# Performance work log

Measured on AMD Instinct MI355X. Metric: run time of the kernel, lower is better.

The kernel has to match this reference:

```python
import jax, jax.numpy as jnp
import numpy as np

N_NODES = 10000
N_EDGES = 320000
S_IN, V_IN = 128, 64          # node irreps 128x0e + 64x1e
ATTR, NB = 64, 32             # node-attr scalars, radial basis size
HEADS, SH, VH = 4, 32, 16     # heads, scalars/head, l=1 vectors/head
FC = 64
S_TP, V_TP = S_IN + V_IN, S_IN + 2 * V_IN   # dtp out: 192x0e + 256x1e
NW = 2 * S_IN + 3 * V_IN                    # 448 TP path weights


def _smooth_leaky(x, alpha=0.2):
    return 0.5 * (1 + alpha) * x + 0.5 * (1 - alpha) * x * (2 * jax.nn.sigmoid(x) - 1)


def _dtp(s, v, y0, y1, w):
    """Depthwise CG tensor product of (s:0e, v:1e) with sh (y0:0e, y1:1e).
    w: [E, 448] per-edge weights or [448] internal weights."""
    w_ss = w[..., :S_IN]
    w_sv = w[..., S_IN:2 * S_IN]
    w_vs = w[..., 2 * S_IN:2 * S_IN + V_IN]
    w_dt = w[..., 2 * S_IN + V_IN:2 * S_IN + 2 * V_IN]
    w_cr = w[..., 2 * S_IN + 2 * V_IN:]
    o0a = w_ss * s * y0                                   # 0e x 0e -> 0e
    o0b = w_dt * jnp.einsum('eci,ei->ec', v, y1)          # 1e . 1e -> 0e
    o1a = (w_sv * s)[:, :, None] * y1[:, None, :]         # 0e x 1e -> 1e
    o1b = w_vs[..., None] * v * y0[:, :, None]            # 1e x 0e -> 1e
    o1c = w_cr[..., None] * jnp.cross(v, jnp.broadcast_to(y1[:, None, :], v.shape))  # 1e x 1e -> 1e
    return jnp.concatenate([o0a, o0b], -1), jnp.concatenate([o1a, o1b, o1c], 1)


def setup_inputs() -> dict:
    key = jax.random.key(0)
    ks = jax.random.split(key, 32)
    g = lambda i, shape, scale=1.0: (jax.random.normal(ks[i], shape, jnp.float32) * scale)
    inv = lambda n: 1.0 / np.sqrt(n)
    FIN = NB + 2 * ATTR
    GATE_S = S_IN + V_IN
    inp = {}
    inp['node_input'] = g(0, (N_NODES, S_IN + 3 * V_IN))
    inp['node_attr'] = g(1, (N_NODES, ATTR))
    inp['edge_attr'] = g(2, (N_EDGES, 4))
    inp['edge_embedding'] = g(3, (N_EDGES, NB))
    inp['edge_src'] = jax.random.randint(ks[4], (N_EDGES,), 0, N_NODES)
    inp['edge_dst'] = jax.random.randint(ks[5], (N_EDGES,), 0, N_NODES)
    inp['W_src_s'] = g(6, (S_IN, S_IN), inv(S_IN)); inp['b_src_s'] = jnp.zeros(S_IN)
    inp['W_src_v'] = g(7, (V_IN, V_IN), inv(V_IN))
    inp['W_dst_s'] = g(8, (S_IN, S_IN), inv(S_IN))
    inp['W_dst_v'] = g(9, (V_IN, V_IN), inv(V_IN))
    inp['rad_W0'] = g(10, (FIN, FC), inv(FIN)); inp['rad_b0'] = jnp.zeros(FC)
    inp['rad_W1'] = g(11, (FC, FC), inv(FC)); inp['rad_b1'] = jnp.zeros(FC)
    inp['rad_W2'] = g(12, (FC, NW), inv(FC)); inp['rad_b2'] = jnp.zeros(NW)
    inp['lin1_Ws'] = g(13, (S_TP, GATE_S), inv(S_TP)); inp['lin1_bs'] = jnp.zeros(GATE_S)
    inp['lin1_Wv'] = g(14, (V_TP, V_IN), inv(V_TP))
    inp['att_Ws'] = g(15, (S_TP, S_IN), inv(S_TP)); inp['att_bs'] = jnp.zeros(S_IN)
    inp['tp2_w'] = g(16, (NW,), 1.0)
    inp['lin2_Ws'] = g(17, (S_TP, S_IN), inv(S_TP)); inp['lin2_bs'] = jnp.zeros(S_IN)
    inp['lin2_Wv'] = g(18, (V_TP, V_IN), inv(V_TP))
    inp['attention_dot'] = g(19, (HEADS, SH), inv(SH))
    inp['out_Ws'] = g(20, (S_IN, S_IN), inv(S_IN)); inp['out_bs'] = jnp.zeros(S_IN)
    inp['out_Wv'] = g(21, (V_IN, V_IN), inv(V_IN))
    return inp


def reference(node_input, node_attr, edge_src, edge_dst, edge_attr, edge_embedding,
              W_src_s, b_src_s, W_src_v, W_dst_s, W_dst_v,
              rad_W0, rad_b0, rad_W1, rad_b1, rad_W2, rad_b2,
              lin1_Ws, lin1_bs, lin1_Wv, att_Ws, att_bs, tp2_w,
              lin2_Ws, lin2_bs, lin2_Wv, attention_dot, out_Ws, out_bs, out_Wv):
    n = node_input.shape[0]
    s = node_input[:, :S_IN]
    v = node_input[:, S_IN:].reshape(n, V_IN, 3)
    y0, y1 = edge_attr[:, :1], edge_attr[:, 1:4]
    # LinearRS src/dst projections (per-irrep channel mixing; bias only on scalars of src)
    ms = s @ W_src_s + b_src_s
    mv = jnp.einsum('nci,cd->ndi', v, W_src_v)
    ds = s @ W_dst_s
    dv = jnp.einsum('nci,cd->ndi', v, W_dst_v)
    es = ms[edge_src] + ds[edge_dst]                      # [E, 128]
    ev = mv[edge_src] + dv[edge_dst]                      # [E, 64, 3]
    # radial MLP on [edge_embedding, src_attr, dst_attr] -> TP weights
    wf = jnp.concatenate([edge_embedding, node_attr[edge_src], node_attr[edge_dst]], -1)
    h = jax.nn.silu(wf @ rad_W0 + rad_b0)
    h = jax.nn.silu(h @ rad_W1 + rad_b1)
    w = h @ rad_W2 + rad_b2                               # [E, 448]
    s_tp, v_tp = _dtp(es, ev, y0, y1, w)                  # [E,192], [E,256,3]
    # attention scores from TP scalars
    sc = s_tp @ att_Ws + att_bs                           # [E, 128]
    # gated linear back to pre-attn irreps
    gs = s_tp @ lin1_Ws + lin1_bs                         # [E, 192]
    gv = jnp.einsum('eci,cd->edi', v_tp, lin1_Wv)         # [E, 64, 3]
    fs = jax.nn.silu(gs[:, :S_IN])
    fv = gv * jax.nn.sigmoid(gs[:, S_IN:])[:, :, None]
    # value net: internal-weight TP + linear to heads irreps
    s2, v2 = _dtp(fs, fv, y0, y1, tp2_w)
    val_s = s2 @ lin2_Ws + lin2_bs                        # [E, 128]
    val_v = jnp.einsum('eci,cd->edi', v2, lin2_Wv)        # [E, 64, 3]
    e = sc.shape[0]
    a = _smooth_leaky(sc.reshape(e, HEADS, SH))
    logits = jnp.einsum('ehk,hk->eh', a, attention_dot)
    # segment softmax over edges sharing the same destination node
    m = jax.ops.segment_max(logits, edge_dst, num_segments=n)
    z = jnp.exp(logits - m[edge_dst])
    den = jax.ops.segment_sum(z, edge_dst, num_segments=n)
    alpha = z / (den[edge_dst] + 1e-12)                   # [E, H]
    out_s = jax.ops.segment_sum(val_s.reshape(e, HEADS, SH) * alpha[..., None],
                                edge_dst, num_segments=n).reshape(n, S_IN)
    out_v = jax.ops.segment_sum(val_v.reshape(e, HEADS, VH, 3) * alpha[..., None, None],
                                edge_dst, num_segments=n).reshape(n, V_IN, 3)
    fo_s = out_s @ out_Ws + out_bs
    fo_v = jnp.einsum('nci,cd->ndi', out_v, out_Wv)
    return jnp.concatenate([fo_s, fo_v.reshape(n, 3 * V_IN)], -1)
```

## Files before the change

### kernel.cpp

```cpp
#include <hip/hip_runtime.h>

#define TE 8
#define NT 16

__device__ __forceinline__ float sigm(float x){ return 1.f / (1.f + __expf(-x)); }
__device__ __forceinline__ float siluf(float x){ return x / (1.f + __expf(-x)); }
__device__ __forceinline__ void atomAddF(float* p, float v){
  __hip_atomic_fetch_add(p, v, __ATOMIC_RELAXED, __HIP_MEMORY_SCOPE_AGENT);
}

template<int EC>
__device__ __forceinline__ void ldact(const float* p, float* av){
  if constexpr (EC >= 4){
    #pragma unroll
    for (int q = 0; q < EC/4; ++q){
      float4 t = *reinterpret_cast<const float4*>(p + 4*q);
      av[4*q+0]=t.x; av[4*q+1]=t.y; av[4*q+2]=t.z; av[4*q+3]=t.w;
    }
  } else if constexpr (EC == 2){
    float2 t = *reinterpret_cast<const float2*>(p);
    av[0]=t.x; av[1]=t.y;
  } else {
    av[0]=*p;
  }
}

__device__ __forceinline__ void ldw2(const float* W, int off, float* wv){
  float2 w = *reinterpret_cast<const float2*>(W + off);
  wv[0] = w.x; wv[1] = w.y;
}

template<int TILE, int K, int N, int NJ, int EG, class WL, class Post>
__device__ __forceinline__ void gemv_t(const float* pool, int actOff, int vtid,
                                       WL wload, Post post){
  constexpr int JT = N / NJ;
  constexpr int EC = TILE / EG;
  constexpr int ACT = JT * EG;
  static_assert(N % NJ == 0 && TILE % EG == 0, "bad cfg");
  if ((unsigned)vtid >= (unsigned)ACT) return;
  const int jt = vtid % JT, g = vtid / JT;
  const int j0 = jt * NJ, eb = g * EC;
  float acc[EC][NJ];
  #pragma unroll
  for (int e = 0; e < EC; ++e){
    #pragma unroll
    for (int t = 0; t < NJ; ++t) acc[e][t] = 0.f;
  }
  const float* ap = pool + actOff*TILE + eb;
  #pragma unroll 4
  for (int k = 0; k < K; ++k){
    float av[EC]; ldact<EC>(ap + k*TILE, av);
    float wv[NJ]; wload(k, j0, wv);
    #pragma unroll
    for (int t = 0; t < NJ; ++t){
      #pragma unroll
      for (int e = 0; e < EC; ++e)
        acc[e][t] = fmaf(av[e], wv[t], acc[e][t]);
    }
  }
  #pragma unroll
  for (int t = 0; t < NJ; ++t){
    #pragma unroll
    for (int e = 0; e < EC; ++e)
      post(j0 + t, eb + e, acc[e][t]);
  }
}

__global__ __launch_bounds__(256) void k_node_pre(
    const float* __restrict__ node_input,
    const float* __restrict__ Wss, const float* __restrict__ bss,
    const float* __restrict__ Wsv,
    const float* __restrict__ Wds, const float* __restrict__ Wdv,
    float* __restrict__ msA, float* __restrict__ dsA,
    float* __restrict__ mvA, float* __restrict__ dvA)
{
  __shared__ __align__(16) float pl[320*NT];
  float* PL = pl;
  const int tid = threadIdx.x;
  const int n0 = blockIdx.x * NT;
  {
    int e = tid & 15, p = tid >> 4;
    const float* row = node_input + (size_t)(n0 + e)*320;
    for (int c = p; c < 128; c += 16) pl[c*NT + e] = row[c];
    for (int c = p; c < 64; c += 16){
      pl[(128 +       c)*NT + e] = row[128 + c*3 + 0];
      pl[(128 + 64  + c)*NT + e] = row[128 + c*3 + 1];
      pl[(128 + 128 + c)*NT + e] = row[128 + c*3 + 2];
    }
  }
  __syncthreads();
  gemv_t<NT,128,128,2,4>(PL, 0, tid,
    [=](int k,int j0,float* wv){ ldw2(Wss, k*128 + j0, wv); },
    [=](int j,int e,float v){ msA[(size_t)(n0+e)*128 + j] = bss[j] + v; });
  gemv_t<NT,128,128,2,4>(PL, 0, tid,
    [=](int k,int j0,float* wv){ ldw2(Wds, k*128 + j0, wv); },
    [=](int j,int e,float v){ dsA[(size_t)(n0+e)*128 + j] = v; });
  #pragma unroll
  for (int i = 0; i < 3; ++i){
    gemv_t<NT,64,64,2,8>(PL, 128 + i*64, tid,
      [=](int k,int j0,float* wv){ ldw2(Wsv, k*64 + j0, wv); },
      [=](int j,int e,float v){ mvA[(size_t)(n0+e)*192 + i*64 + j] = v; });
    gemv_t<NT,64,64,2,8>(PL, 128 + i*64, tid,
      [=](int k,int j0,float* wv){ ldw2(Wdv, k*64 + j0, wv); },
      [=](int j,int e,float v){ dvA[(size_t)(n0+e)*192 + i*64 + j] = v; });
  }
}

__global__ __launch_bounds__(256, 4) void k_edge(
    const float* __restrict__ edge_attr, const float* __restrict__ edge_emb,
    const int* __restrict__ esrc, const int* __restrict__ edst,
    const float* __restrict__ node_attr,
    const float* __restrict__ msA, const float* __restrict__ dsA,
    const float* __restrict__ mvA, const float* __restrict__ dvA,
    const float* __restrict__ rW0, const float* __restrict__ rb0,
    const float* __restrict__ rW1, const float* __restrict__ rb1,
    const float* __restrict__ rW2, const float* __restrict__ rb2,
    const float* __restrict__ l1Ws, const float* __restrict__ l1bs, const float* __restrict__ l1Wv,
    const float* __restrict__ aWs, const float* __restrict__ abs_, const float* __restrict__ adot,
    const float* __restrict__ tp2w,
    const float* __restrict__ l2Ws, const float* __restrict__ l2bs, const float* __restrict__ l2Wv,
    float* __restrict__ den, float* __restrict__ num_s, float* __restrict__ num_v)
{
  constexpr int O_EV  = 0;
  constexpr int O_S2  = 0;
  constexpr int O_WF  = 192;
  constexpr int O_STP = 192;
  constexpr int O_GV  = 192;
  constexpr int O_CRW = 384;
  constexpr int O_FCR = 384;
  constexpr int O_ES  = 576;
  constexpr int O_GSA = 576;
  constexpr int O_T1A = 704;
  constexpr int O_U1B = 704;
  constexpr int O_H2  = 832;
  constexpr int O_T1  = 832;
  constexpr int O_H1  = 896;
  constexpr int O_GSB = 896;

  __shared__ __align__(16) float pool[960*TE];
  __shared__ float y0s[TE], y1s[3*TE], zl[4*TE], lg[4*TE];
  __shared__ int srcI[TE], dstI[TE];

  float* PL = pool;
  float* ZL = zl;
  float* Y0 = y0s;
  int*   DI = dstI;

  const int tid = threadIdx.x;
  const int e0 = blockIdx.x * TE;

  if (tid < TE){ srcI[tid] = esrc[e0 + tid]; dstI[tid] = edst[e0 + tid]; }
  if (tid < 4*TE){
    int e = tid >> 2, q = tid & 3;
    float v = edge_attr[(size_t)(e0 + e)*4 + q];
    if (q == 0) y0s[e] = v; else y1s[(q-1)*TE + e] = v;
  }
  __syncthreads();

  {
    int e = tid & 7, p = tid >> 3;
    int si = srcI[e], di = dstI[e];
    for (int c = p; c < 160; c += 32){
      float v;
      if (c < 32)       v = edge_emb[(size_t)(e0+e)*32 + c];
      else if (c < 96)  v = node_attr[(size_t)si*64 + (c-32)];
      else              v = node_attr[(size_t)di*64 + (c-96)];
      pool[(O_WF + c)*TE + e] = v;
    }
  }
  __syncthreads();

  if (tid < 128){
    gemv_t<TE,160,64,1,2>(PL, O_WF, tid,
      [=](int k,int j0,float* wv){ wv[0] = rW0[k*64 + j0]; },
      [=](int j,int e,float v){ PL[(O_H1 + j)*TE + e] = siluf(rb0[j] + v); });
  } else if (tid < 192){
    int r = tid - 128, e = r & 7, p = r >> 3;
    const float* mp = msA + (size_t)srcI[e]*128;
    const float* dp = dsA + (size_t)dstI[e]*128;
    int c0 = p*16;
    #pragma unroll
    for (int q = 0; q < 4; ++q){
      float4 m = *reinterpret_cast<const float4*>(mp + c0 + q*4);
      float4 d = *reinterpret_cast<const float4*>(dp + c0 + q*4);
      pool[(O_ES + c0 + q*4 + 0)*TE + e] = m.x + d.x;
      pool[(O_ES + c0 + q*4 + 1)*TE + e] = m.y + d.y;
      pool[(O_ES + c0 + q*4 + 2)*TE + e] = m.z + d.z;
      pool[(O_ES + c0 + q*4 + 3)*TE + e] = m.w + d.w;
    }
  } else {
    int r = tid - 192, e = r & 7, p = r >> 3;
    const float* mp = mvA + (size_t)srcI[e]*192;
    const float* dp = dvA + (size_t)dstI[e]*192;
    int c0 = p*8;
    #pragma unroll
    for (int i = 0; i < 3; ++i){
      #pragma unroll
      for (int q = 0; q < 2; ++q){
        float4 m = *reinterpret_cast<const float4*>(mp + i*64 + c0 + q*4);
        float4 d = *reinterpret_cast<const float4*>(dp + i*64 + c0 + q*4);
        pool[(O_EV + i*64 + c0 + q*4 + 0)*TE + e] = m.x + d.x;
        pool[(O_EV + i*64 + c0 + q*4 + 1)*TE + e] = m.y + d.y;
        pool[(O_EV + i*64 + c0 + q*4 + 2)*TE + e] = m.z + d.z;
        pool[(O_EV + i*64 + c0 + q*4 + 3)*TE + e] = m.w + d.w;
      }
    }
  }
  __syncthreads();

  if (tid < 128){
    gemv_t<TE,64,64,1,2>(PL, O_H1, tid,
      [=](int k,int j0,float* wv){ wv[0] = rW1[k*64 + j0]; },
      [=](int j,int e,float v){ PL[(O_H2 + j)*TE + e] = siluf(rb1[j] + v); });
  }
  __syncthreads();

  if (tid < 128){
    gemv_t<TE,64,128,1,1>(PL, O_H2, tid,
      [=](int k,int j0,float* wv){ wv[0] = rW2[k*448 + 128 + j0]; },
      [=](int j,int e,float v){
        PL[(O_T1A + j)*TE + e] = (rb2[128 + j] + v) * PL[(O_ES + j)*TE + e];
      });
  } else if (tid < 192){
    gemv_t<TE,64,128,2,1>(PL, O_H2, tid - 128,
      [=](int k,int j0,float* wv){ ldw2(rW2, k*448 + j0, wv); },
      [=](int j,int e,float v){
        PL[(O_STP + j)*TE + e] = (rb2[j] + v) * PL[(O_ES + j)*TE + e] * Y0[e];
      });
  } else {
    int c = tid - 192;
    float avs[TE], adt[TE], acr[TE];
    #pragma unroll
    for (int e = 0; e < TE; ++e){ avs[e]=0.f; adt[e]=0.f; acr[e]=0.f; }
    const float* hp = PL + O_H2*TE;
    #pragma unroll 4
    for (int k = 0; k < 64; ++k){
      float av[TE]; ldact<TE>(hp + k*TE, av);
      float wv = rW2[k*448 + 256 + c];
      float wd = rW2[k*448 + 320 + c];
      float wc = rW2[k*448 + 384 + c];
      #pragma unroll
      for (int e = 0; e < TE; ++e){
        avs[e] = fmaf(av[e], wv, avs[e]);
        adt[e] = fmaf(av[e], wd, adt[e]);
        acr[e] = fmaf(av[e], wc, acr[e]);
      }
    }
    float bvs = rb2[256+c], bdt = rb2[320+c], bcr = rb2[384+c];
    #pragma unroll
    for (int e = 0; e < TE; ++e){
      float wvs = avs[e]+bvs, wdt = adt[e]+bdt, wcr = acr[e]+bcr;
      float ev0 = pool[(O_EV +       c)*TE + e];
      float ev1 = pool[(O_EV + 64  + c)*TE + e];
      float ev2 = pool[(O_EV + 128 + c)*TE + e];
      float y10 = y1s[e], y11 = y1s[TE + e], y12 = y1s[2*TE + e];
      pool[(O_STP + 128 + c)*TE + e] = wdt * (ev0*y10 + ev1*y11 + ev2*y12);
      pool[(O_EV +       c)*TE + e] = wvs * ev0;
      pool[(O_EV + 64  + c)*TE + e] = wvs * ev1;
      pool[(O_EV + 128 + c)*TE + e] = wvs * ev2;
      pool[(O_CRW +       c)*TE + e] = wcr * (ev1*y12 - ev2*y11);
      pool[(O_CRW + 64  + c)*TE + e] = wcr * (ev2*y10 - ev0*y12);
      pool[(O_CRW + 128 + c)*TE + e] = wcr * (ev0*y11 - ev1*y10);
    }
  }
  __syncthreads();

  if (tid < 128){
    int j = tid;
    float acc[TE];
    #pragma unroll
    for (int e = 0; e < TE; ++e) acc[e] = 0.f;
    const float* ap = PL + O_STP*TE;
    #pragma unroll 4
    for (int k = 0; k < 192; ++k){
      float av[TE]; ldact<TE>(ap + k*TE, av);
      float w = aWs[k*128 + j];
      #pragma unroll
      for (int e = 0; e < TE; ++e) acc[e] = fmaf(av[e], w, acc[e]);
    }
    float bb = abs_[j], dt = adot[j];
    int h = j >> 5;
    #pragma unroll
    for (int e = 0; e < TE; ++e){
      float t = acc[e] + bb;
      float c = t * (0.2f + 0.8f*sigm(t)) * dt;
      c += __shfl_xor(c, 1, 32);
      c += __shfl_xor(c, 2, 32);
      c += __shfl_xor(c, 4, 32);
      c += __shfl_xor(c, 8, 32);
      c += __shfl_xor(c, 16, 32);
      if ((j & 31) == 0) lg[h*TE + e] = c;
    }
  } else if (tid < 192){
    gemv_t<TE,192,64,1,1>(PL, O_STP, tid - 128,
      [=](int k,int j0,float* wv){ wv[0] = l1Ws[k*192 + 128 + j0]; },
      [=](int j,int e,float v){ PL[(O_GSB + j)*TE + e] = sigm(l1bs[128 + j] + v); });
  } else {
    gemv_t<TE,128,64,1,1>(PL, O_T1A, tid - 192,
      [=](int k,int j0,float* wv){ wv[0] = l1Wv[k*64 + j0]; },
      [=](int j,int e,float v){ PL[(O_T1 + j)*TE + e] = v; });
  }
  __syncthreads();

  gemv_t<TE,192,128,1,2>(PL, O_STP, tid,
    [=](int k,int j0,float* wv){ wv[0] = l1Ws[k*192 + j0]; },
    [=](int j,int e,float v){ PL[(O_GSA + j)*TE + e] = siluf(l1bs[j] + v); });
  __syncthreads();

  if (tid < 192){
    int i = tid >> 6, d = tid & 63;
    float accP[TE], accY[TE];
    #pragma unroll
    for (int e = 0; e < TE; ++e){
      accP[e] = y1s[i*TE + e] * pool[(O_T1 + d)*TE + e];
      accY[e] = 0.f;
    }
    #pragma unroll 2
    for (int k = 0; k < 64; ++k){
      float av[TE], cv[TE];
      ldact<TE>(&pool[(O_EV  + i*64 + k)*TE], av);
      ldact<TE>(&pool[(O_CRW + i*64 + k)*TE], cv);
      float w2 = l1Wv[(128 + k)*64 + d];
      float w3 = l1Wv[(192 + k)*64 + d];
      #pragma unroll
      for (int e = 0; e < TE; ++e){
        accY[e] = fmaf(av[e], w2, accY[e]);
        accP[e] = fmaf(cv[e], w3, accP[e]);
      }
    }
    #pragma unroll
    for (int e = 0; e < TE; ++e){
      float val = accP[e] + y0s[e]*accY[e];
      pool[(O_GV + i*64 + d)*TE + e] = val * pool[(O_GSB + d)*TE + e];
    }
  } else {
    gemv_t<TE,128,64,1,1>(PL, O_GSA, tid - 192,
      [=](int k,int j0,float* wv){ wv[0] = tp2w[128 + k] * l2Wv[k*64 + j0]; },
      [=](int j,int e,float v){ PL[(O_U1B + j)*TE + e] = v; });
  }
  __syncthreads();

  if (tid < 128){
    int e = tid & 7, p = tid >> 3;
    float yy0 = y0s[e];
    float y10 = y1s[e], y11 = y1s[TE + e], y12 = y1s[2*TE + e];
    for (int c = p; c < 128; c += 16){
      pool[(O_S2 + c)*TE + e] = tp2w[c] * pool[(O_GSA + c)*TE + e] * yy0;
    }
    for (int c = p; c < 64; c += 16){
      float f0 = pool[(O_GV +       c)*TE + e];
      float f1 = pool[(O_GV + 64  + c)*TE + e];
      float f2 = pool[(O_GV + 128 + c)*TE + e];
      pool[(O_S2 + 128 + c)*TE + e] = tp2w[320 + c] * (f0*y10 + f1*y11 + f2*y12);
      pool[(O_FCR +       c)*TE + e] = f1*y12 - f2*y11;
      pool[(O_FCR + 64  + c)*TE + e] = f2*y10 - f0*y12;
      pool[(O_FCR + 128 + c)*TE + e] = f0*y11 - f1*y10;
    }
  } else if (tid < 160){
    int r = tid - 128, e = r & 7, h = r >> 3;
    float z = __expf(lg[h*TE + e]);
    zl[h*TE + e] = z;
    atomAddF(&den[(size_t)dstI[e]*4 + h], z);
  }
  __syncthreads();

  if (tid < 128){
    gemv_t<TE,192,128,1,1>(PL, O_S2, tid,
      [=](int k,int j0,float* wv){ wv[0] = l2Ws[k*128 + j0]; },
      [=](int j,int e,float v){
        float vv = (l2bs[j] + v) * ZL[(j >> 5)*TE + e];
        atomAddF(&num_s[(size_t)DI[e]*128 + j], vv);
      });
  } else if (tid < 224){
    int r = tid - 128;
    int i = r / 32, d0 = (r % 32) * 2;
    float accP[TE][2], accY[TE][2];
    #pragma unroll
    for (int e = 0; e < TE; ++e){
      float y1v = y1s[i*TE + e];
      accP[e][0] = y1v * pool[(O_U1B + d0    )*TE + e];
      accP[e][1] = y1v * pool[(O_U1B + d0 + 1)*TE + e];
      accY[e][0] = 0.f; accY[e][1] = 0.f;
    }
    #pragma unroll 2
    for (int k = 0; k < 64; ++k){
      float av[TE], cv[TE];
      ldact<TE>(&pool[(O_GV  + i*64 + k)*TE], av);
      ldact<TE>(&pool[(O_FCR + i*64 + k)*TE], cv);
      float w2[2], w3[2];
      float s2c = tp2w[256 + k];
      float s3c = tp2w[384 + k];
      ldw2(l2Wv, (128 + k)*64 + d0, w2);
      ldw2(l2Wv, (192 + k)*64 + d0, w3);
      w2[0]*=s2c; w2[1]*=s2c; w3[0]*=s3c; w3[1]*=s3c;
      #pragma unroll
      for (int e = 0; e < TE; ++e){
        accY[e][0] = fmaf(av[e], w2[0], accY[e][0]);
        accY[e][1] = fmaf(av[e], w2[1], accY[e][1]);
        accP[e][0] = fmaf(cv[e], w3[0], accP[e][0]);
        accP[e][1] = fmaf(cv[e], w3[1], accP[e][1]);
      }
    }
    #pragma unroll
    for (int t = 0; t < 2; ++t){
      int d = d0 + t;
      int h = d >> 4;
      #pragma unroll
      for (int e = 0; e < TE; ++e){
        float val = accP[e][t] + y0s[e]*accY[e][t];
        atomAddF(&num_v[(size_t)dstI[e]*192 + i*64 + d], val * zl[h*TE + e]);
      }
    }
  }
}

__global__ __launch_bounds__(256) void k_node_out(
    const float* __restrict__ den, const float* __restrict__ num_s, const float* __restrict__ num_v,
    const float* __restrict__ Wos, const float* __restrict__ bos, const float* __restrict__ Wov,
    float* __restrict__ out)
{
  __shared__ __align__(16) float pl[320*NT];
  __shared__ float dl[4*NT];
  float* PL = pl;
  const int tid = threadIdx.x;
  const int n0 = blockIdx.x * NT;
  if (tid < 64){
    int e = tid & 15, h = tid >> 4;
    dl[h*NT + e] = den[(size_t)(n0 + e)*4 + h] + 1e-12f;
  }
  __syncthreads();
  {
    int e = tid & 15, p = tid >> 4;
    for (int c = p; c < 128; c += 16)
      pl[c*NT + e] = num_s[(size_t)(n0+e)*128 + c] / dl[(c >> 5)*NT + e];
    for (int c = p; c < 64; c += 16){
      float dd = dl[(c >> 4)*NT + e];
      pl[(128 +       c)*NT + e] = num_v[(size_t)(n0+e)*192 +       c] / dd;
      pl[(128 + 64  + c)*NT + e] = num_v[(size_t)(n0+e)*192 + 64  + c] / dd;
      pl[(128 + 128 + c)*NT + e] = num_v[(size_t)(n0+e)*192 + 128 + c] / dd;
    }
  }
  __syncthreads();
  gemv_t<NT,128,128,2,4>(PL, 0, tid,
    [=](int k,int j0,float* wv){ ldw2(Wos, k*128 + j0, wv); },
    [=](int j,int e,float v){ out[(size_t)(n0+e)*320 + j] = bos[j] + v; });
  #pragma unroll
  for (int i = 0; i < 3; ++i){
    gemv_t<NT,64,64,2,8>(PL, 128 + i*64, tid,
      [=](int k,int j0,float* wv){ ldw2(Wov, k*64 + j0, wv); },
      [=](int j,int e,float v){ out[(size_t)(n0+e)*320 + 128 + j*3 + i] = v; });
  }
}

extern "C" void kernel_launch(void* const* d_in, const int* in_sizes, int n_in,
                              void* d_out, int out_size, void* d_ws, size_t ws_size,
                              hipStream_t stream)
{
  const float* node_input = (const float*)d_in[0];
  const float* node_attr  = (const float*)d_in[1];
  const float* edge_attr  = (const float*)d_in[2];
  const float* edge_emb   = (const float*)d_in[3];
  const int* edge_src   = (const int*)d_in[4];
  const int* edge_dst   = (const int*)d_in[5];
  const float* W_src_s = (const float*)d_in[6];
  const float* b_src_s = (const float*)d_in[7];
  const float* W_src_v = (const float*)d_in[8];
  const float* W_dst_s = (const float*)d_in[9];
  const float* W_dst_v = (const float*)d_in[10];
  const float* rad_W0  = (const float*)d_in[11];
  const float* rad_b0  = (const float*)d_in[12];
  const float* rad_W1  = (const float*)d_in[13];
  const float* rad_b1  = (const float*)d_in[14];
  const float* rad_W2  = (const float*)d_in[15];
  const float* rad_b2  = (const float*)d_in[16];
  const float* lin1_Ws = (const float*)d_in[17];
  const float* lin1_bs = (const float*)d_in[18];
  const float* lin1_Wv = (const float*)d_in[19];
  const float* att_Ws  = (const float*)d_in[20];
  const float* att_bs  = (const float*)d_in[21];
  const float* tp2_w   = (const float*)d_in[22];
  const float* lin2_Ws = (const float*)d_in[23];
  const float* lin2_bs = (const float*)d_in[24];
  const float* lin2_Wv = (const float*)d_in[25];
  const float* att_dot = (const float*)d_in[26];
  const float* out_Ws  = (const float*)d_in[27];
  const float* out_bs  = (const float*)d_in[28];
  const float* out_Wv  = (const float*)d_in[29];

  const int nN = in_sizes[0] / 320;
  const int nE = in_sizes[4];

  float* ws    = (float*)d_ws;
  float* den   = ws;
  float* num_s = den   + (size_t)nN * 4;
  float* num_v = num_s + (size_t)nN * 128;
  float* msA   = num_v + (size_t)nN * 192;
  float* dsA   = msA   + (size_t)nN * 128;
  float* mvA   = dsA   + (size_t)nN * 128;
  float* dvA   = mvA   + (size_t)nN * 192;

  size_t need = ((size_t)nN * (4 + 128 + 192 + 128 + 128 + 192 + 192)) * sizeof(float);
  if (ws_size < need) return;

  hipMemsetAsync(den, 0, (size_t)nN * (4 + 128 + 192) * sizeof(float), stream);

  k_node_pre<<<nN/NT, 256, 0, stream>>>(node_input, W_src_s, b_src_s, W_src_v,
                                        W_dst_s, W_dst_v, msA, dsA, mvA, dvA);
  k_edge<<<nE/TE, 256, 0, stream>>>(edge_attr, edge_emb, edge_src, edge_dst, node_attr,
                                    msA, dsA, mvA, dvA,
                                    rad_W0, rad_b0, rad_W1, rad_b1, rad_W2, rad_b2,
                                    lin1_Ws, lin1_bs, lin1_Wv,
                                    att_Ws, att_bs, att_dot,
                                    tp2_w, lin2_Ws, lin2_bs, lin2_Wv,
                                    den, num_s, num_v);
  k_node_out<<<nN/NT, 256, 0, stream>>>(den, num_s, num_v, out_Ws, out_bs, out_Wv,
                                        (float*)d_out);
}
```

Baseline: 2.467 ms.

## Rebalance edge-kernel thread work across stages and overlap value-net GEMV with TP prep

Redistributes work inside the per-edge-tile kernel so all 256 threads participate in the radial MLP and attention-score GEMVs. Idle threads previously waited at barriers, and the attention GEMV now splits edges across two thread groups. The value-net scalar GEMV is split into two phases: the first consumes the gated scalars directly (folding tp2w into the weights) while other threads build the dot/cross-product tensors. The l=1 accumulation is split the same way, which shortens the serial stage chain. This adds one barrier and keeps accumulators live across stages, which raises register pressure.

```diff
diff --git a/kernel.cpp b/kernel.cpp
--- a/kernel.cpp
+++ b/kernel.cpp
@@ -122,7 +122,6 @@
     float* __restrict__ den, float* __restrict__ num_s, float* __restrict__ num_v)
 {
   constexpr int O_EV  = 0;
-  constexpr int O_S2  = 0;
   constexpr int O_WF  = 192;
   constexpr int O_STP = 192;
   constexpr int O_GV  = 192;
@@ -134,6 +133,7 @@
   constexpr int O_U1B = 704;
   constexpr int O_H2  = 832;
   constexpr int O_T1  = 832;
+  constexpr int O_DV  = 832;
   constexpr int O_H1  = 896;
   constexpr int O_GSB = 896;
 
@@ -208,39 +208,38 @@
   }
   __syncthreads();
 
-  if (tid < 128){
-    gemv_t<TE,64,64,1,2>(PL, O_H1, tid,
-      [=](int k,int j0,float* wv){ wv[0] = rW1[k*64 + j0]; },
-      [=](int j,int e,float v){ PL[(O_H2 + j)*TE + e] = siluf(rb1[j] + v); });
-  }
-  __syncthreads();
-
-  if (tid < 128){
-    gemv_t<TE,64,128,1,1>(PL, O_H2, tid,
-      [=](int k,int j0,float* wv){ wv[0] = rW2[k*448 + 128 + j0]; },
+  gemv_t<TE,64,64,1,4>(PL, O_H1, tid,
+    [=](int k,int j0,float* wv){ wv[0] = rW1[k*64 + j0]; },
+    [=](int j,int e,float v){ PL[(O_H2 + j)*TE + e] = siluf(rb1[j] + v); });
+  __syncthreads();
+
+  if (tid < 64){
+    gemv_t<TE,64,128,2,1>(PL, O_H2, tid,
+      [=](int k,int j0,float* wv){ ldw2(rW2, k*448 + 128 + j0, wv); },
       [=](int j,int e,float v){
         PL[(O_T1A + j)*TE + e] = (rb2[128 + j] + v) * PL[(O_ES + j)*TE + e];
       });
-  } else if (tid < 192){
-    gemv_t<TE,64,128,2,1>(PL, O_H2, tid - 128,
+  } else if (tid < 128){
+    gemv_t<TE,64,128,2,1>(PL, O_H2, tid - 64,
       [=](int k,int j0,float* wv){ ldw2(rW2, k*448 + j0, wv); },
       [=](int j,int e,float v){
         PL[(O_STP + j)*TE + e] = (rb2[j] + v) * PL[(O_ES + j)*TE + e] * Y0[e];
       });
   } else {
-    int c = tid - 192;
-    float avs[TE], adt[TE], acr[TE];
-    #pragma unroll
-    for (int e = 0; e < TE; ++e){ avs[e]=0.f; adt[e]=0.f; acr[e]=0.f; }
-    const float* hp = PL + O_H2*TE;
+    int r = tid - 128, c = r & 63, g = r >> 6;
+    int eb = g * 4;
+    float avs[4], adt[4], acr[4];
+    #pragma unroll
+    for (int e = 0; e < 4; ++e){ avs[e]=0.f; adt[e]=0.f; acr[e]=0.f; }
+    const float* hp = PL + O_H2*TE + eb;
     #pragma unroll 4
     for (int k = 0; k < 64; ++k){
-      float av[TE]; ldact<TE>(hp + k*TE, av);
+      float av[4]; ldact<4>(hp + k*TE, av);
       float wv = rW2[k*448 + 256 + c];
       float wd = rW2[k*448 + 320 + c];
       float wc = rW2[k*448 + 384 + c];
       #pragma unroll
-      for (int e = 0; e < TE; ++e){
+      for (int e = 0; e < 4; ++e){
         avs[e] = fmaf(av[e], wv, avs[e]);
         adt[e] = fmaf(av[e], wd, adt[e]);
         acr[e] = fmaf(av[e], wc, acr[e]);
@@ -248,40 +247,39 @@
     }
     float bvs = rb2[256+c], bdt = rb2[320+c], bcr = rb2[384+c];
     #pragma unroll
-    for (int e = 0; e < TE; ++e){
+    for (int e = 0; e < 4; ++e){
+      int ee = eb + e;
       float wvs = avs[e]+bvs, wdt = adt[e]+bdt, wcr = acr[e]+bcr;
-      float ev0 = pool[(O_EV +       c)*TE + e];
-      float ev1 = pool[(O_EV + 64  + c)*TE + e];
-      float ev2 = pool[(O_EV + 128 + c)*TE + e];
-      float y10 = y1s[e], y11 = y1s[TE + e], y12 = y1s[2*TE + e];
-      pool[(O_STP + 128 + c)*TE + e] = wdt * (ev0*y10 + ev1*y11 + ev2*y12);
-      pool[(O_EV +       c)*TE + e] = wvs * ev0;
-      pool[(O_EV + 64  + c)*TE + e] = wvs * ev1;
-      pool[(O_EV + 128 + c)*TE + e] = wvs * ev2;
-      pool[(O_CRW +       c)*TE + e] = wcr * (ev1*y12 - ev2*y11);
-      pool[(O_CRW + 64  + c)*TE + e] = wcr * (ev2*y10 - ev0*y12);
-      pool[(O_CRW + 128 + c)*TE + e] = wcr * (ev0*y11 - ev1*y10);
-    }
-  }
-  __syncthreads();
-
-  if (tid < 128){
-    int j = tid;
-    float acc[TE];
-    #pragma unroll
-    for (int e = 0; e < TE; ++e) acc[e] = 0.f;
-    const float* ap = PL + O_STP*TE;
+      float ev0 = pool[(O_EV +       c)*TE + ee];
+      float ev1 = pool[(O_EV + 64  + c)*TE + ee];
+      float ev2 = pool[(O_EV + 128 + c)*TE + ee];
+      float y10 = y1s[ee], y11 = y1s[TE + ee], y12 = y1s[2*TE + ee];
+      pool[(O_STP + 128 + c)*TE + ee] = wdt * (ev0*y10 + ev1*y11 + ev2*y12);
+      pool[(O_EV +       c)*TE + ee] = wvs * ev0;
+      pool[(O_EV + 64  + c)*TE + ee] = wvs * ev1;
+      pool[(O_EV + 128 + c)*TE + ee] = wvs * ev2;
+      pool[(O_CRW +       c)*TE + ee] = wcr * (ev1*y12 - ev2*y11);
+      pool[(O_CRW + 64  + c)*TE + ee] = wcr * (ev2*y10 - ev0*y12);
+      pool[(O_CRW + 128 + c)*TE + ee] = wcr * (ev0*y11 - ev1*y10);
+    }
+  }
+  __syncthreads();
+
+  {
+    int j = tid & 127, g = tid >> 7, eb = g*4;
+    float acc[4] = {0.f,0.f,0.f,0.f};
+    const float* ap = PL + O_STP*TE + eb;
     #pragma unroll 4
     for (int k = 0; k < 192; ++k){
-      float av[TE]; ldact<TE>(ap + k*TE, av);
+      float av[4]; ldact<4>(ap + k*TE, av);
       float w = aWs[k*128 + j];
       #pragma unroll
-      for (int e = 0; e < TE; ++e) acc[e] = fmaf(av[e], w, acc[e]);
+      for (int e = 0; e < 4; ++e) acc[e] = fmaf(av[e], w, acc[e]);
     }
     float bb = abs_[j], dt = adot[j];
     int h = j >> 5;
     #pragma unroll
-    for (int e = 0; e < TE; ++e){
+    for (int e = 0; e < 4; ++e){
       float t = acc[e] + bb;
       float c = t * (0.2f + 0.8f*sigm(t)) * dt;
       c += __shfl_xor(c, 1, 32);
@@ -289,14 +287,17 @@
       c += __shfl_xor(c, 4, 32);
       c += __shfl_xor(c, 8, 32);
       c += __shfl_xor(c, 16, 32);
-      if ((j & 31) == 0) lg[h*TE + e] = c;
-    }
-  } else if (tid < 192){
-    gemv_t<TE,192,64,1,1>(PL, O_STP, tid - 128,
+      if ((j & 31) == 0) lg[h*TE + eb + e] = c;
+    }
+  }
+  __syncthreads();
+
+  if (tid < 128){
+    gemv_t<TE,192,64,1,2>(PL, O_STP, tid,
       [=](int k,int j0,float* wv){ wv[0] = l1Ws[k*192 + 128 + j0]; },
       [=](int j,int e,float v){ PL[(O_GSB + j)*TE + e] = sigm(l1bs[128 + j] + v); });
   } else {
-    gemv_t<TE,128,64,1,1>(PL, O_T1A, tid - 192,
+    gemv_t<TE,128,64,1,2>(PL, O_T1A, tid - 128,
       [=](int k,int j0,float* wv){ wv[0] = l1Wv[k*64 + j0]; },
       [=](int j,int e,float v){ PL[(O_T1 + j)*TE + e] = v; });
   }
@@ -340,63 +341,99 @@
   }
   __syncthreads();
 
+  float vsacc[TE];
+  float vvY[TE][2];
+
   if (tid < 128){
-    int e = tid & 7, p = tid >> 3;
-    float yy0 = y0s[e];
-    float y10 = y1s[e], y11 = y1s[TE + e], y12 = y1s[2*TE + e];
-    for (int c = p; c < 128; c += 16){
-      pool[(O_S2 + c)*TE + e] = tp2w[c] * pool[(O_GSA + c)*TE + e] * yy0;
-    }
-    for (int c = p; c < 64; c += 16){
-      float f0 = pool[(O_GV +       c)*TE + e];
-      float f1 = pool[(O_GV + 64  + c)*TE + e];
-      float f2 = pool[(O_GV + 128 + c)*TE + e];
-      pool[(O_S2 + 128 + c)*TE + e] = tp2w[320 + c] * (f0*y10 + f1*y11 + f2*y12);
-      pool[(O_FCR +       c)*TE + e] = f1*y12 - f2*y11;
-      pool[(O_FCR + 64  + c)*TE + e] = f2*y10 - f0*y12;
-      pool[(O_FCR + 128 + c)*TE + e] = f0*y11 - f1*y10;
-    }
-  } else if (tid < 160){
-    int r = tid - 128, e = r & 7, h = r >> 3;
-    float z = __expf(lg[h*TE + e]);
-    zl[h*TE + e] = z;
-    atomAddF(&den[(size_t)dstI[e]*4 + h], z);
-  }
-  __syncthreads();
-
-  if (tid < 128){
-    gemv_t<TE,192,128,1,1>(PL, O_S2, tid,
-      [=](int k,int j0,float* wv){ wv[0] = l2Ws[k*128 + j0]; },
-      [=](int j,int e,float v){
-        float vv = (l2bs[j] + v) * ZL[(j >> 5)*TE + e];
-        atomAddF(&num_s[(size_t)DI[e]*128 + j], vv);
-      });
+    int j = tid;
+    #pragma unroll
+    for (int e = 0; e < TE; ++e) vsacc[e] = 0.f;
+    const float* ap = PL + O_GSA*TE;
+    #pragma unroll 2
+    for (int k = 0; k < 128; ++k){
+      float av[TE]; ldact<TE>(ap + k*TE, av);
+      float w = tp2w[k] * l2Ws[k*128 + j];
+      #pragma unroll
+      for (int e = 0; e < TE; ++e) vsacc[e] = fmaf(av[e], w, vsacc[e]);
+    }
+    #pragma unroll
+    for (int e = 0; e < TE; ++e) vsacc[e] *= y0s[e];
   } else if (tid < 224){
     int r = tid - 128;
     int i = r / 32, d0 = (r % 32) * 2;
-    float accP[TE][2], accY[TE][2];
+    #pragma unroll
+    for (int e = 0; e < TE; ++e){ vvY[e][0] = 0.f; vvY[e][1] = 0.f; }
+    #pragma unroll 2
+    for (int k = 0; k < 64; ++k){
+      float av[TE]; ldact<TE>(&pool[(O_GV + i*64 + k)*TE], av);
+      float w2[2];
+      float s2c = tp2w[256 + k];
+      ldw2(l2Wv, (128 + k)*64 + d0, w2);
+      w2[0]*=s2c; w2[1]*=s2c;
+      #pragma unroll
+      for (int e = 0; e < TE; ++e){
+        vvY[e][0] = fmaf(av[e], w2[0], vvY[e][0]);
+        vvY[e][1] = fmaf(av[e], w2[1], vvY[e][1]);
+      }
+    }
+  } else {
+    {
+      int r = tid - 224, e = r & 7, p = r >> 3;
+      float y10 = y1s[e], y11 = y1s[TE + e], y12 = y1s[2*TE + e];
+      for (int c = p; c < 64; c += 4){
+        float f0 = pool[(O_GV +       c)*TE + e];
+        float f1 = pool[(O_GV + 64  + c)*TE + e];
+        float f2 = pool[(O_GV + 128 + c)*TE + e];
+        pool[(O_DV + c)*TE + e]        = f0*y10 + f1*y11 + f2*y12;
+        pool[(O_FCR +       c)*TE + e] = f1*y12 - f2*y11;
+        pool[(O_FCR + 64  + c)*TE + e] = f2*y10 - f0*y12;
+        pool[(O_FCR + 128 + c)*TE + e] = f0*y11 - f1*y10;
+      }
+    }
+    {
+      int r = tid - 224, e = r & 7, h = r >> 3;
+      float z = __expf(lg[h*TE + e]);
+      zl[h*TE + e] = z;
+      atomAddF(&den[(size_t)dstI[e]*4 + h], z);
+    }
+  }
+  __syncthreads();
+
+  if (tid < 128){
+    int j = tid;
+    #pragma unroll 2
+    for (int k = 0; k < 64; ++k){
+      float av[TE]; ldact<TE>(&pool[(O_DV + k)*TE], av);
+      float w = tp2w[320 + k] * l2Ws[(128 + k)*128 + j];
+      #pragma unroll
+      for (int e = 0; e < TE; ++e) vsacc[e] = fmaf(av[e], w, vsacc[e]);
+    }
+    float bb = l2bs[j];
+    int hs = j >> 5;
+    #pragma unroll
+    for (int e = 0; e < TE; ++e){
+      float vv = (vsacc[e] + bb) * ZL[hs*TE + e];
+      atomAddF(&num_s[(size_t)DI[e]*128 + j], vv);
+    }
+  } else if (tid < 224){
+    int r = tid - 128;
+    int i = r / 32, d0 = (r % 32) * 2;
+    float accP[TE][2];
     #pragma unroll
     for (int e = 0; e < TE; ++e){
       float y1v = y1s[i*TE + e];
       accP[e][0] = y1v * pool[(O_U1B + d0    )*TE + e];
       accP[e][1] = y1v * pool[(O_U1B + d0 + 1)*TE + e];
-      accY[e][0] = 0.f; accY[e][1] = 0.f;
     }
     #pragma unroll 2
     for (int k = 0; k < 64; ++k){
-      float av[TE], cv[TE];
-      ldact<TE>(&pool[(O_GV  + i*64 + k)*TE], av);
-      ldact<TE>(&pool[(O_FCR + i*64 + k)*TE], cv);
-      float w2[2], w3[2];
-      float s2c = tp2w[256 + k];
+      float cv[TE]; ldact<TE>(&pool[(O_FCR + i*64 + k)*TE], cv);
+      float w3[2];
       float s3c = tp2w[384 + k];
-      ldw2(l2Wv, (128 + k)*64 + d0, w2);
       ldw2(l2Wv, (192 + k)*64 + d0, w3);
-      w2[0]*=s2c; w2[1]*=s2c; w3[0]*=s3c; w3[1]*=s3c;
+      w3[0]*=s3c; w3[1]*=s3c;
       #pragma unroll
       for (int e = 0; e < TE; ++e){
-        accY[e][0] = fmaf(av[e], w2[0], accY[e][0]);
-        accY[e][1] = fmaf(av[e], w2[1], accY[e][1]);
         accP[e][0] = fmaf(cv[e], w3[0], accP[e][0]);
         accP[e][1] = fmaf(cv[e], w3[1], accP[e][1]);
       }
@@ -407,7 +444,7 @@
       int h = d >> 4;
       #pragma unroll
       for (int e = 0; e < TE; ++e){
-        float val = accP[e][t] + y0s[e]*accY[e][t];
+        float val = accP[e][t] + y0s[e]*vvY[e][t];
         atomAddF(&num_v[(size_t)dstI[e]*192 + i*64 + d], val * zl[h*TE + e]);
       }
     }
```

Measured after the change: 2.754 ms. 11.6% more time.
